# Optimization experiments

Measured on AMD Instinct MI355X. Metric: run time of the kernel, lower is better.

## Reference

```python
import jax, jax.numpy as jnp
import numpy as np

B = 65536
L = 200
NUM_VARS = 2
NUM_PARAMS = 7
EPS = 1e-12


def setup_inputs() -> dict:
    key = jax.random.key(0)
    transformer_out = jax.random.normal(key, (B, NUM_PARAMS * NUM_VARS, 1), dtype=jnp.float32)
    return {"transformer_out": transformer_out}


def reference(transformer_out):
    # transformer_out: (B, 14, 1). chunk(num_vars, dim=1) -> two (B,7,1) slices; take [:,:,0].
    b = transformer_out.shape[0]
    p = transformer_out[:, :, 0].reshape(b, NUM_VARS, NUM_PARAMS)  # (B, V, 7)
    lam = 0.001 * jax.nn.relu(p[..., 0])          # (B, V)
    beta = 1.0 + 10.0 * jax.nn.relu(p[..., 1])
    k_d = p[..., 2]
    mu = p[..., 3]
    k_f = p[..., 4]
    n_c = p[..., 5]
    w_t = p[..., 6]

    def step(carry, n):
        D, F = carry
        one_minus_D = jnp.maximum(1.0 - D, EPS)
        D = jnp.minimum(D + lam * jnp.exp(beta * jnp.log(one_minus_D)), 1.0 - EPS)
        g = jax.nn.sigmoid((n - n_c) / w_t)
        F = jnp.clip((1.0 + mu * g) * F + EPS * g, 0.0, 1.0 - EPS)
        deltaR = k_d * D + k_f * F
        return (D, F), deltaR

    init = (jnp.zeros_like(lam), jnp.full_like(lam, EPS))
    steps = jnp.arange(L, dtype=transformer_out.dtype)
    _, ys = jax.lax.scan(step, init, steps)  # ys: (L, B, V)
    # per-var output is (B, L); torch cats the V chunks along last dim -> (B, V*L)
    return jnp.transpose(ys, (1, 2, 0)).reshape(b, NUM_VARS * L)
```

## Files before the change

### kernel.cpp

```cpp
#include <hip/hip_runtime.h>


#if __has_builtin(__builtin_amdgcn_exp2f)
#define FAST_EXP2(x) __builtin_amdgcn_exp2f(x)
#else
#define FAST_EXP2(x) exp2f(x)
#endif
#if __has_builtin(__builtin_amdgcn_logf)
#define FAST_LOG2(x) __builtin_amdgcn_logf(x)
#else
#define FAST_LOG2(x) log2f(x)
#endif

namespace {
constexpr int kL = 200;
constexpr int kChunk = 20;
constexpr int kNChunk = kL / kChunk;
constexpr float kEps = 1e-12f;
constexpr float kLog2e = 1.44269504088896340736f;
}

__global__ __launch_bounds__(256) void ist_sim_kernel(
    const float* __restrict__ p, float* __restrict__ out) {
  const int tid = blockIdx.x * 256 + threadIdx.x;

  const float* q = p + tid * 7;
  const float lam  = 0.001f * fmaxf(q[0], 0.0f);
  const float beta = fmaf(10.0f, fmaxf(q[1], 0.0f), 1.0f);
  const float kd = q[2];
  const float mu = q[3];
  const float kf = q[4];
  const float nc = q[5];
  const float wt = q[6];

  const float inv_wt = __builtin_amdgcn_rcpf(wt);
  const float a2 = inv_wt * kLog2e;
  const float c2 = nc * a2;

  float D = 0.0f;
  float F = kEps;
  float* o = out + (size_t)tid * kL;

  for (int ch = 0; ch < kNChunk; ++ch) {
    float buf[kChunk];
#pragma unroll
    for (int i = 0; i < kChunk; ++i) {
      const float nf = (float)(ch * kChunk + i);

      const float om = fmaxf(1.0f - D, kEps);
      const float t = beta * FAST_LOG2(om);
      D = fminf(fmaf(lam, FAST_EXP2(t), D), 1.0f);

      const float x2 = fmaf(nf, a2, -c2);
      const float e = FAST_EXP2(-x2);
      const float g = __builtin_amdgcn_rcpf(1.0f + e);

      float v = fmaf(mu * g, F, F);
      v = fmaf(kEps, g, v);
      F = fminf(fmaxf(v, 0.0f), 1.0f);

      buf[i] = fmaf(kd, D, kf * F);
    }
    float4* dst = reinterpret_cast<float4*>(o + ch * kChunk);
#pragma unroll
    for (int j = 0; j < kChunk / 4; ++j) {
      dst[j] = make_float4(buf[4 * j], buf[4 * j + 1], buf[4 * j + 2],
                           buf[4 * j + 3]);
    }
  }
}

extern "C" void kernel_launch(void* const* d_in, const int* in_sizes, int n_in,
                              void* d_out, int out_size, void* d_ws,
                              size_t ws_size, hipStream_t stream) {
  const float* p = (const float*)d_in[0];
  float* out = (float*)d_out;
  const int total_chains = 65536 * 2;
  ist_sim_kernel<<<total_chains / 256, 256, 0, stream>>>(p, out);
}
```

Before: 130.8 us.

## Stage full per-chain outputs in LDS and write coalesced rows

Each thread now computes all 200 steps into a register array instead of working in 20-step chunks. Each wave in turn transposes its results through an XOR-swizzled LDS tile, and the whole block then writes that tile to global memory as contiguous float2 stores. This replaces the strided per-thread float4 stores, where lanes sat 800 bytes apart, with coalesced writes. The cost is about 200 live values per thread, which risks register pressure or spills, plus 64KB of LDS per block, lower occupancy (launch bounds raised to 2 blocks) and four serialized barrier rounds per block.

```diff
diff --git a/kernel.cpp b/kernel.cpp
--- a/kernel.cpp
+++ b/kernel.cpp
@@ -14,15 +14,17 @@
 
 namespace {
 constexpr int kL = 200;
-constexpr int kChunk = 20;
-constexpr int kNChunk = kL / kChunk;
 constexpr float kEps = 1e-12f;
 constexpr float kLog2e = 1.44269504088896340736f;
+constexpr int kRowDw = 256;
 }
 
-__global__ __launch_bounds__(256) void ist_sim_kernel(
+__global__ __launch_bounds__(256, 2) void ist_sim_kernel(
     const float* __restrict__ p, float* __restrict__ out) {
-  const int tid = blockIdx.x * 256 + threadIdx.x;
+  __shared__ float lds[64 * kRowDw];
+
+  const int t = threadIdx.x;
+  const int tid = blockIdx.x * 256 + t;
 
   const float* q = p + tid * 7;
   const float lam  = 0.001f * fmaxf(q[0], 0.0f);
@@ -33,39 +35,50 @@
   const float nc = q[5];
   const float wt = q[6];
 
-  const float inv_wt = __builtin_amdgcn_rcpf(wt);
-  const float a2 = inv_wt * kLog2e;
+  const float a2 = __builtin_amdgcn_rcpf(wt) * kLog2e;
   const float c2 = nc * a2;
 
   float D = 0.0f;
   float F = kEps;
-  float* o = out + (size_t)tid * kL;
+  float buf[kL];
 
-  for (int ch = 0; ch < kNChunk; ++ch) {
-    float buf[kChunk];
 #pragma unroll
-    for (int i = 0; i < kChunk; ++i) {
-      const float nf = (float)(ch * kChunk + i);
+  for (int n = 0; n < kL; ++n) {
+    const float om = fmaxf(1.0f - D, kEps);
+    D = fminf(fmaf(lam, FAST_EXP2(beta * FAST_LOG2(om)), D), 1.0f);
 
-      const float om = fmaxf(1.0f - D, kEps);
-      const float t = beta * FAST_LOG2(om);
-      D = fminf(fmaf(lam, FAST_EXP2(t), D), 1.0f);
+    const float x2 = fmaf((float)n, a2, -c2);
+    const float g = __builtin_amdgcn_rcpf(1.0f + FAST_EXP2(-x2));
 
-      const float x2 = fmaf(nf, a2, -c2);
-      const float e = FAST_EXP2(-x2);
-      const float g = __builtin_amdgcn_rcpf(1.0f + e);
+    float v = fmaf(mu * g, F, F);
+    v = fmaf(kEps, g, v);
+    F = fminf(fmaxf(v, 0.0f), 1.0f);
 
-      float v = fmaf(mu * g, F, F);
-      v = fmaf(kEps, g, v);
-      F = fminf(fmaxf(v, 0.0f), 1.0f);
+    buf[n] = fmaf(kd, D, kf * F);
+  }
 
-      buf[i] = fmaf(kd, D, kf * F);
+  const int wave = t >> 6;
+  const int lane = t & 63;
+  for (int k = 0; k < 4; ++k) {
+    __syncthreads();
+    if (wave == k) {
+#pragma unroll
+      for (int j = 0; j < kL / 2; ++j) {
+        const int dw = lane * kRowDw + 2 * (j ^ (lane & 31));
+        *reinterpret_cast<float2*>(&lds[dw]) =
+            make_float2(buf[2 * j], buf[2 * j + 1]);
+      }
     }
-    float4* dst = reinterpret_cast<float4*>(o + ch * kChunk);
+    __syncthreads();
+    float* gbase = out + ((size_t)blockIdx.x * 256 + (size_t)k * 64) * kL;
 #pragma unroll
-    for (int j = 0; j < kChunk / 4; ++j) {
-      dst[j] = make_float4(buf[4 * j], buf[4 * j + 1], buf[4 * j + 2],
-                           buf[4 * j + 3]);
+    for (int i = 0; i < 25; ++i) {
+      const int f2 = i * 256 + t;
+      const int row = f2 / 100;
+      const int sl = f2 - row * 100;
+      const int dw = row * kRowDw + 2 * (sl ^ (row & 31));
+      const float2 val = *reinterpret_cast<const float2*>(&lds[dw]);
+      *reinterpret_cast<float2*>(&gbase[(size_t)f2 * 2]) = val;
     }
   }
 }
```

New measurement: 124.7 us. 1.05x faster.

## Stage outputs through LDS to coalesce global stores across chains

Applied to the files above, without the earlier changes.

Each wave now writes its per-step results into a padded shared-memory tile and then reads them back transposed, so consecutive lanes store consecutive float4s of the same output row. This replaces the previous pattern where each lane wrote its own strided row. The chunk size doubles to 40 to fit the staging layout. The change costs extra LDS traffic and about 41KB of shared memory per block, which may reduce occupancy.

```diff
diff --git a/kernel.cpp b/kernel.cpp
--- a/kernel.cpp
+++ b/kernel.cpp
@@ -14,15 +14,23 @@
 
 namespace {
 constexpr int kL = 200;
-constexpr int kChunk = 20;
+constexpr int kChunk = 40;
 constexpr int kNChunk = kL / kChunk;
+constexpr int kS = 65;
 constexpr float kEps = 1e-12f;
 constexpr float kLog2e = 1.44269504088896340736f;
 }
 
 __global__ __launch_bounds__(256) void ist_sim_kernel(
     const float* __restrict__ p, float* __restrict__ out) {
-  const int tid = blockIdx.x * 256 + threadIdx.x;
+  __shared__ float lds[4 * kChunk * kS];
+
+  const int t = threadIdx.x;
+  const int lane = t & 63;
+  const int wave = t >> 6;
+  float* wlds = lds + wave * kChunk * kS;
+
+  const int tid = blockIdx.x * 256 + t;
 
   const float* q = p + tid * 7;
   const float lam  = 0.001f * fmaxf(q[0], 0.0f);
@@ -33,39 +41,45 @@
   const float nc = q[5];
   const float wt = q[6];
 
-  const float inv_wt = __builtin_amdgcn_rcpf(wt);
-  const float a2 = inv_wt * kLog2e;
+  const float a2 = __builtin_amdgcn_rcpf(wt) * kLog2e;
   const float c2 = nc * a2;
 
   float D = 0.0f;
   float F = kEps;
-  float* o = out + (size_t)tid * kL;
+
+  float* gbase =
+      out + ((size_t)blockIdx.x * 256 + (size_t)wave * 64) * kL;
 
   for (int ch = 0; ch < kNChunk; ++ch) {
-    float buf[kChunk];
 #pragma unroll
     for (int i = 0; i < kChunk; ++i) {
       const float nf = (float)(ch * kChunk + i);
 
       const float om = fmaxf(1.0f - D, kEps);
-      const float t = beta * FAST_LOG2(om);
-      D = fminf(fmaf(lam, FAST_EXP2(t), D), 1.0f);
+      D = fminf(fmaf(lam, FAST_EXP2(beta * FAST_LOG2(om)), D), 1.0f);
 
       const float x2 = fmaf(nf, a2, -c2);
-      const float e = FAST_EXP2(-x2);
-      const float g = __builtin_amdgcn_rcpf(1.0f + e);
+      const float g = __builtin_amdgcn_rcpf(1.0f + FAST_EXP2(-x2));
 
       float v = fmaf(mu * g, F, F);
       v = fmaf(kEps, g, v);
       F = fminf(fmaxf(v, 0.0f), 1.0f);
 
-      buf[i] = fmaf(kd, D, kf * F);
+      wlds[i * kS + lane] = fmaf(kd, D, kf * F);
     }
-    float4* dst = reinterpret_cast<float4*>(o + ch * kChunk);
+
 #pragma unroll
-    for (int j = 0; j < kChunk / 4; ++j) {
-      dst[j] = make_float4(buf[4 * j], buf[4 * j + 1], buf[4 * j + 2],
-                           buf[4 * j + 3]);
+    for (int it = 0; it < 10; ++it) {
+      const int f = it * 64 + lane;
+      const int c = f / 10;
+      const int s = f - c * 10;
+      float4 v;
+      v.x = wlds[(4 * s + 0) * kS + c];
+      v.y = wlds[(4 * s + 1) * kS + c];
+      v.z = wlds[(4 * s + 2) * kS + c];
+      v.w = wlds[(4 * s + 3) * kS + c];
+      *reinterpret_cast<float4*>(gbase + (size_t)c * kL + ch * kChunk +
+                                 s * 4) = v;
     }
   }
 }
```

New measurement: 124.4 us. 1.05x faster.
